# Performance work log

Hardware: AMD Instinct MI355X
Metric: run time of the kernel (lower is better)

Reference implementation:

```python
import jax, jax.numpy as jnp
from jax import lax
import numpy as np

B, C_IN, C_OUT, T, N, E = 4, 32, 32, 48, 2000, 16000


def _tconv(x, w, b):
    # Conv2d with kernel (3,1), padding (1,0): temporal conv over T, per-node.
    y = lax.conv_general_dilated(x, w, window_strides=(1, 1),
                                 padding=((1, 1), (0, 0)),
                                 dimension_numbers=('NCHW', 'OIHW', 'NCHW'))
    return y + b[None, :, None, None]


def setup_inputs() -> dict:
    key = jax.random.key(0)
    ks = jax.random.split(key, 8)
    x = jax.random.normal(ks[0], (B, C_IN, T, N), dtype=jnp.float32)
    edge_index = jax.random.randint(ks[1], (2, E), 0, N, dtype=jnp.int64)
    w1 = jax.random.normal(ks[2], (C_OUT, C_IN, 3, 1), dtype=jnp.float32) * 0.05
    b1 = jnp.zeros((C_OUT,), dtype=jnp.float32)
    gcn_w = jax.random.normal(ks[3], (C_OUT, C_OUT), dtype=jnp.float32) * 0.05
    gcn_b = jnp.zeros((C_OUT,), dtype=jnp.float32)
    w2 = jax.random.normal(ks[4], (C_OUT, C_OUT, 3, 1), dtype=jnp.float32) * 0.05
    b2 = jnp.zeros((C_OUT,), dtype=jnp.float32)
    return {"x": x, "edge_index": edge_index, "w1": w1, "b1": b1,
            "gcn_w": gcn_w, "gcn_b": gcn_b, "w2": w2, "b2": b2}


def reference(x, edge_index, w1, b1, gcn_w, gcn_b, w2, b2):
    # temporal conv 1 + relu
    h = jax.nn.relu(_tconv(x, w1, b1))          # [B, C, T, N]
    Bs, C, Ts, Ns = h.shape
    # replicate-graph GCN: same edge_index for all B*T graphs
    xf = h.transpose(0, 2, 3, 1).reshape(Bs * Ts, Ns, C)   # [BT, N, C]
    xw = xf @ gcn_w                                        # linear transform first
    src, dst = edge_index[0], edge_index[1]
    # GCN symmetric normalization with self-loops: deg = 1 + in-degree
    deg = jnp.zeros((Ns,), xw.dtype).at[dst].add(1.0) + 1.0
    dinv = lax.rsqrt(deg)
    wedge = dinv[src] * dinv[dst]                           # [E]

    def aggregate(g):  # g: [N, C] for one graph
        return jnp.zeros((Ns, C), g.dtype).at[dst].add(g[src] * wedge[:, None])

    agg = jax.vmap(aggregate)(xw)                           # [BT, N, C]
    out = agg + (1.0 / deg)[None, :, None] * xw + gcn_b     # self-loop term + bias
    out = out.reshape(Bs, Ts, Ns, C).transpose(0, 3, 1, 2)  # [B, C, T, N]
    # temporal conv 2
    return _tconv(out, w2, b2)
```

## Files before the change

### kernel.cpp

```cpp
#include <hip/hip_runtime.h>

#define BB 4
#define CIN 32
#define COUT 32
#define TT 48
#define NN 2000
#define EE 16000
#define BT (BB*TT)
#define PADCOL 24576
#define NGB 24


__global__ __launch_bounds__(1024) void k_build(
        const int* __restrict__ ei,
        const float* __restrict__ w1, const float* __restrict__ gw,
        const float* __restrict__ gb, const float* __restrict__ w2,
        int* __restrict__ rowptr, float* __restrict__ dinv2,
        int* __restrict__ col, float* __restrict__ wedge,
        float* __restrict__ w1t, float* __restrict__ w2c,
        float* __restrict__ bias2) {
    __shared__ int   cnt[2048];
    __shared__ int   buf[2048];
    __shared__ float sdinv[2048];
    __shared__ float sw2t[3072];
    __shared__ float sgw[1024];
    int t = threadIdx.x;

    for (int i = t; i < 3072; i += 1024) {
        int c = i & 31, r = i >> 5;
        int co = r & 31, k = r >> 5;
        sw2t[i] = w2[c * 96 + co * 3 + k];
        w1t[i]  = w1[c * 96 + co * 3 + k];
    }
    sgw[t] = gw[t];
    cnt[t] = 0; cnt[t + 1024] = 0;
    __syncthreads();

    for (int e = t; e < EE; e += 1024) atomicAdd(&cnt[ei[EE + e]], 1);
    __syncthreads();

    for (int i = t; i < 2048; i += 1024)
        buf[i] = (i < NN) ? ((cnt[i] + 3) & ~3) : 0;
    __syncthreads();
    for (int s = 1; s < 2048; s <<= 1) {
        int i0 = t, i1 = t + 1024;
        int a0 = buf[i0] + ((i0 >= s) ? buf[i0 - s] : 0);
        int a1 = buf[i1] + ((i1 >= s) ? buf[i1 - s] : 0);
        __syncthreads();
        buf[i0] = a0; buf[i1] = a1;
        __syncthreads();
    }

    for (int i = t; i < 2048; i += 1024) {
        if (i < NN) {
            rowptr[i + 1] = buf[i];
            float deg = (float)(cnt[i] + 1);
            sdinv[i] = rsqrtf(deg);
            dinv2[i] = 1.0f / deg;
        }
    }
    if (t == 0) rowptr[0] = 0;
    __syncthreads();

    int P = buf[NN - 1];
    for (int i = t; i < P; i += 1024) { col[i] = 0; wedge[i] = 0.f; }
    for (int i = t; i < NN; i += 1024)
        cnt[i] = buf[i] - ((cnt[i] + 3) & ~3);
    __syncthreads();

    for (int e = t; e < EE; e += 1024) {
        int s = ei[e], d = ei[EE + e];
        int pos = atomicAdd(&cnt[d], 1);
        col[pos]   = s;
        wedge[pos] = sdinv[s] * sdinv[d];
    }

    for (int i = t; i < 3072; i += 1024) {
        int c = i & 31, r = i >> 5;
        int cm = r & 31, k = r >> 5;
        float acc = 0.f;
#pragma unroll
        for (int co = 0; co < 32; co++)
            acc += sgw[cm * 32 + co] * sw2t[(k * 32 + co) * 32 + c];
        w2c[i] = acc;
    }
    for (int i = t; i < 96; i += 1024) {
        int k = i >> 5, c = i & 31;
        float acc = 0.f;
#pragma unroll
        for (int co = 0; co < 32; co++)
            acc += gb[co] * sw2t[(k * 32 + co) * 32 + c];
        bias2[i] = acc;
    }
}


__global__ __launch_bounds__(256) void k_conv1(const float* __restrict__ x,
                                               const float* __restrict__ w1t,
                                               const float* __restrict__ b1,
                                               float* __restrict__ hbuf) {
    int idx = blockIdx.x * 256 + threadIdx.x;
    int n0 = idx * 2;
    if (n0 >= NN) return;
    int t = blockIdx.y, b = blockIdx.z;
    int g = b * TT + t;
    int gb = g >> 3, gsub = g & 7;

    float ha[COUT], hb[COUT];
#pragma unroll
    for (int c = 0; c < COUT; c++) { ha[c] = b1[c]; hb[c] = b1[c]; }

    for (int k = 0; k < 3; k++) {
        int tt = t + k - 1;
        if (tt < 0 || tt >= TT) continue;
        const float* xb = x + (((size_t)b * CIN) * TT + tt) * NN + n0;
        const float* wp = w1t + k * CIN * COUT;
#pragma unroll
        for (int ci = 0; ci < CIN; ci++) {
            float2 xv = *(const float2*)(xb + (size_t)ci * TT * NN);
#pragma unroll
            for (int c = 0; c < COUT; c++) {
                float wv = wp[ci * COUT + c];
                ha[c] += xv.x * wv;
                hb[c] += xv.y * wv;
            }
        }
    }

    float4* pa = (float4*)(hbuf + (((size_t)gb * NN + n0) * 8 + gsub) * 32);
    float4* pb = (float4*)(hbuf + (((size_t)gb * NN + n0 + 1) * 8 + gsub) * 32);
#pragma unroll
    for (int q = 0; q < 8; q++) {
        pa[q] = make_float4(fmaxf(ha[4*q], 0.f), fmaxf(ha[4*q+1], 0.f),
                            fmaxf(ha[4*q+2], 0.f), fmaxf(ha[4*q+3], 0.f));
        pb[q] = make_float4(fmaxf(hb[4*q], 0.f), fmaxf(hb[4*q+1], 0.f),
                            fmaxf(hb[4*q+2], 0.f), fmaxf(hb[4*q+3], 0.f));
    }
}


__global__ __launch_bounds__(256) void k_agg(const float* __restrict__ hbuf,
                                             const int* __restrict__ rowptr,
                                             const int* __restrict__ col,
                                             const float* __restrict__ wedge,
                                             const float* __restrict__ dinv2,
                                             float* __restrict__ gbuf) {
    int bid = blockIdx.x;
    int xcd = bid & 7;
    int q   = bid >> 3;
    int gbr = q / 500;
    int nch = q % 500;
    int gb  = gbr * 8 + xcd;
    int wid  = threadIdx.x >> 6;
    int lane = threadIdx.x & 63;
    int gsub = lane >> 3;
    int cq   = lane & 7;
    int n    = nch * 4 + wid;

    const float* xg = hbuf + (size_t)gb * NN * 256;
    size_t loff = (size_t)gsub * 32 + cq * 4;

    float4 self = *(const float4*)(xg + (size_t)n * 256 + loff);
    float dv = dinv2[n];
    float4 acc = make_float4(dv * self.x, dv * self.y, dv * self.z, dv * self.w);

    int j  = rowptr[n];
    int je = rowptr[n + 1];
    for (; j < je; j += 4) {
        int4   cc = *(const int4*)(col + j);
        float4 ww = *(const float4*)(wedge + j);
        float4 v0 = *(const float4*)(xg + (size_t)cc.x * 256 + loff);
        float4 v1 = *(const float4*)(xg + (size_t)cc.y * 256 + loff);
        float4 v2 = *(const float4*)(xg + (size_t)cc.z * 256 + loff);
        float4 v3 = *(const float4*)(xg + (size_t)cc.w * 256 + loff);
        acc.x += ww.x*v0.x + ww.y*v1.x + ww.z*v2.x + ww.w*v3.x;
        acc.y += ww.x*v0.y + ww.y*v1.y + ww.z*v2.y + ww.w*v3.y;
        acc.z += ww.x*v0.z + ww.y*v1.z + ww.z*v2.z + ww.w*v3.z;
        acc.w += ww.x*v0.w + ww.y*v1.w + ww.z*v2.w + ww.w*v3.w;
    }

    int g = gb * 8 + gsub;
    *(float4*)(gbuf + ((size_t)g * NN + n) * 32 + cq * 4) = acc;
}


__global__ __launch_bounds__(256) void k_conv2(const float* __restrict__ gbuf,
                                               const float* __restrict__ w2c,
                                               const float* __restrict__ bias2,
                                               const float* __restrict__ b2,
                                               float* __restrict__ out) {
    int n = blockIdx.x * 256 + threadIdx.x;
    if (n >= NN) return;
    int t = blockIdx.y, b = blockIdx.z;

    float o[COUT];
#pragma unroll
    for (int c = 0; c < COUT; c++) o[c] = b2[c];

    for (int k = 0; k < 3; k++) {
        int tt = t + k - 1;
        if (tt < 0 || tt >= TT) continue;
        const float4* gp = (const float4*)(gbuf + (((size_t)(b * TT + tt)) * NN + n) * CIN);
        const float* wp = w2c + k * CIN * COUT;
        const float* bp = bias2 + k * COUT;
        float gv[CIN];
#pragma unroll
        for (int qq = 0; qq < 8; qq++) {
            float4 v = gp[qq];
            gv[4*qq] = v.x; gv[4*qq+1] = v.y; gv[4*qq+2] = v.z; gv[4*qq+3] = v.w;
        }
#pragma unroll
        for (int c = 0; c < COUT; c++) o[c] += bp[c];
#pragma unroll
        for (int cm = 0; cm < CIN; cm++) {
#pragma unroll
            for (int c = 0; c < COUT; c++) o[c] += gv[cm] * wp[cm * COUT + c];
        }
    }

#pragma unroll
    for (int c = 0; c < COUT; c++)
        out[(((size_t)b * COUT + c) * TT + t) * NN + n] = o[c];
}


extern "C" void kernel_launch(void* const* d_in, const int* in_sizes, int n_in,
                              void* d_out, int out_size, void* d_ws, size_t ws_size,
                              hipStream_t stream) {
    const float* x     = (const float*)d_in[0];
    const int*   ei    = (const int*)d_in[1];
    const float* w1    = (const float*)d_in[2];
    const float* b1    = (const float*)d_in[3];
    const float* gcn_w = (const float*)d_in[4];
    const float* gcn_b = (const float*)d_in[5];
    const float* w2    = (const float*)d_in[6];
    const float* b2    = (const float*)d_in[7];
    float* out = (float*)d_out;

    const size_t XWB = (size_t)BT * NN * COUT * sizeof(float);
    char* w = (char*)d_ws;
    float* hbuf   = (float*)w;  w += XWB;
    float* gbuf   = (float*)w;  w += XWB;
    int*   rowptr = (int*)w;    w += 8192;
    float* dinv2  = (float*)w;  w += 8192;
    int*   col    = (int*)w;    w += PADCOL * sizeof(int);
    float* wedge  = (float*)w;  w += PADCOL * sizeof(float);
    float* w1t    = (float*)w;  w += 3072 * sizeof(float);
    float* w2c    = (float*)w;  w += 3072 * sizeof(float);
    float* bias2  = (float*)w;  w += 96 * sizeof(float);

    k_build<<<dim3(1), dim3(1024), 0, stream>>>(ei, w1, gcn_w, gcn_b, w2,
                                                rowptr, dinv2, col, wedge,
                                                w1t, w2c, bias2);
    k_conv1<<<dim3(4, TT, BB), dim3(256), 0, stream>>>(x, w1t, b1, hbuf);
    k_agg  <<<dim3(12000), dim3(256), 0, stream>>>(hbuf, rowptr, col, wedge, dinv2, gbuf);
    k_conv2<<<dim3(8, TT, BB), dim3(256), 0, stream>>>(gbuf, w2c, bias2, b2, out);
}
```

Before: 269.1 us.

## Move CSR edge fill to a parallel kernel and use one node per conv1 thread

The edge scatter that fills col/wedge moves out of the single-block build kernel into a separate multi-block kernel that uses global atomics on a fill pointer. The aim is to shorten the serial single-workgroup setup phase. Conv1 now has each thread compute one node instead of two and launches twice as many blocks, which raises parallelism and lowers register pressure but drops the float2 loads. The change adds one kernel launch, and the global atomics make the edge order within each row nondeterministic, as it already was.

```diff
diff --git a/kernel.cpp b/kernel.cpp
--- a/kernel.cpp
+++ b/kernel.cpp
@@ -8,7 +8,6 @@
 #define EE 16000
 #define BT (BB*TT)
 #define PADCOL 24576
-#define NGB 24
 
 
 __global__ __launch_bounds__(1024) void k_build(
@@ -16,12 +15,12 @@
         const float* __restrict__ w1, const float* __restrict__ gw,
         const float* __restrict__ gb, const float* __restrict__ w2,
         int* __restrict__ rowptr, float* __restrict__ dinv2,
+        float* __restrict__ dinvg, int* __restrict__ fillptr,
         int* __restrict__ col, float* __restrict__ wedge,
         float* __restrict__ w1t, float* __restrict__ w2c,
         float* __restrict__ bias2) {
     __shared__ int   cnt[2048];
     __shared__ int   buf[2048];
-    __shared__ float sdinv[2048];
     __shared__ float sw2t[3072];
     __shared__ float sgw[1024];
     int t = threadIdx.x;
@@ -55,25 +54,16 @@
         if (i < NN) {
             rowptr[i + 1] = buf[i];
             float deg = (float)(cnt[i] + 1);
-            sdinv[i] = rsqrtf(deg);
+            dinvg[i] = rsqrtf(deg);
             dinv2[i] = 1.0f / deg;
+            fillptr[i] = buf[i] - ((cnt[i] + 3) & ~3);
         }
     }
     if (t == 0) rowptr[0] = 0;
-    __syncthreads();
 
     int P = buf[NN - 1];
+    __syncthreads();
     for (int i = t; i < P; i += 1024) { col[i] = 0; wedge[i] = 0.f; }
-    for (int i = t; i < NN; i += 1024)
-        cnt[i] = buf[i] - ((cnt[i] + 3) & ~3);
-    __syncthreads();
-
-    for (int e = t; e < EE; e += 1024) {
-        int s = ei[e], d = ei[EE + e];
-        int pos = atomicAdd(&cnt[d], 1);
-        col[pos]   = s;
-        wedge[pos] = sdinv[s] * sdinv[d];
-    }
 
     for (int i = t; i < 3072; i += 1024) {
         int c = i & 31, r = i >> 5;
@@ -95,47 +85,51 @@
 }
 
 
+__global__ void k_fill(const int* __restrict__ ei, int* __restrict__ fillptr,
+                       const float* __restrict__ dinvg,
+                       int* __restrict__ col, float* __restrict__ wedge) {
+    int e = blockIdx.x * blockDim.x + threadIdx.x;
+    if (e < EE) {
+        int s = ei[e], d = ei[EE + e];
+        int pos = atomicAdd(fillptr + d, 1);
+        col[pos]   = s;
+        wedge[pos] = dinvg[s] * dinvg[d];
+    }
+}
+
+
 __global__ __launch_bounds__(256) void k_conv1(const float* __restrict__ x,
                                                const float* __restrict__ w1t,
                                                const float* __restrict__ b1,
                                                float* __restrict__ hbuf) {
-    int idx = blockIdx.x * 256 + threadIdx.x;
-    int n0 = idx * 2;
-    if (n0 >= NN) return;
+    int n = blockIdx.x * 256 + threadIdx.x;
+    if (n >= NN) return;
     int t = blockIdx.y, b = blockIdx.z;
     int g = b * TT + t;
     int gb = g >> 3, gsub = g & 7;
 
-    float ha[COUT], hb[COUT];
-#pragma unroll
-    for (int c = 0; c < COUT; c++) { ha[c] = b1[c]; hb[c] = b1[c]; }
+    float ha[COUT];
+#pragma unroll
+    for (int c = 0; c < COUT; c++) ha[c] = b1[c];
 
     for (int k = 0; k < 3; k++) {
         int tt = t + k - 1;
         if (tt < 0 || tt >= TT) continue;
-        const float* xb = x + (((size_t)b * CIN) * TT + tt) * NN + n0;
+        const float* xb = x + (((size_t)b * CIN) * TT + tt) * NN + n;
         const float* wp = w1t + k * CIN * COUT;
 #pragma unroll
         for (int ci = 0; ci < CIN; ci++) {
-            float2 xv = *(const float2*)(xb + (size_t)ci * TT * NN);
-#pragma unroll
-            for (int c = 0; c < COUT; c++) {
-                float wv = wp[ci * COUT + c];
-                ha[c] += xv.x * wv;
-                hb[c] += xv.y * wv;
-            }
-        }
-    }
-
-    float4* pa = (float4*)(hbuf + (((size_t)gb * NN + n0) * 8 + gsub) * 32);
-    float4* pb = (float4*)(hbuf + (((size_t)gb * NN + n0 + 1) * 8 + gsub) * 32);
-#pragma unroll
-    for (int q = 0; q < 8; q++) {
+            float xv = xb[(size_t)ci * TT * NN];
+#pragma unroll
+            for (int c = 0; c < COUT; c++) ha[c] += xv * wp[ci * COUT + c];
+        }
+    }
+
+    float4* pa = (float4*)(hbuf + (((size_t)gb * NN + n) * 8 + gsub) * 32);
+#pragma unroll
+    for (int q = 0; q < 8; q++)
         pa[q] = make_float4(fmaxf(ha[4*q], 0.f), fmaxf(ha[4*q+1], 0.f),
                             fmaxf(ha[4*q+2], 0.f), fmaxf(ha[4*q+3], 0.f));
-        pb[q] = make_float4(fmaxf(hb[4*q], 0.f), fmaxf(hb[4*q+1], 0.f),
-                            fmaxf(hb[4*q+2], 0.f), fmaxf(hb[4*q+3], 0.f));
-    }
 }
 
 
@@ -239,20 +233,23 @@
 
     const size_t XWB = (size_t)BT * NN * COUT * sizeof(float);
     char* w = (char*)d_ws;
-    float* hbuf   = (float*)w;  w += XWB;
-    float* gbuf   = (float*)w;  w += XWB;
-    int*   rowptr = (int*)w;    w += 8192;
-    float* dinv2  = (float*)w;  w += 8192;
-    int*   col    = (int*)w;    w += PADCOL * sizeof(int);
-    float* wedge  = (float*)w;  w += PADCOL * sizeof(float);
-    float* w1t    = (float*)w;  w += 3072 * sizeof(float);
-    float* w2c    = (float*)w;  w += 3072 * sizeof(float);
-    float* bias2  = (float*)w;  w += 96 * sizeof(float);
+    float* hbuf    = (float*)w;  w += XWB;
+    float* gbuf    = (float*)w;  w += XWB;
+    int*   rowptr  = (int*)w;    w += 8192;
+    float* dinv2   = (float*)w;  w += 8192;
+    float* dinvg   = (float*)w;  w += 8192;
+    int*   fillptr = (int*)w;    w += 8192;
+    int*   col     = (int*)w;    w += PADCOL * sizeof(int);
+    float* wedge   = (float*)w;  w += PADCOL * sizeof(float);
+    float* w1t     = (float*)w;  w += 3072 * sizeof(float);
+    float* w2c     = (float*)w;  w += 3072 * sizeof(float);
+    float* bias2   = (float*)w;  w += 96 * sizeof(float);
 
     k_build<<<dim3(1), dim3(1024), 0, stream>>>(ei, w1, gcn_w, gcn_b, w2,
-                                                rowptr, dinv2, col, wedge,
-                                                w1t, w2c, bias2);
-    k_conv1<<<dim3(4, TT, BB), dim3(256), 0, stream>>>(x, w1t, b1, hbuf);
+                                                rowptr, dinv2, dinvg, fillptr,
+                                                col, wedge, w1t, w2c, bias2);
+    k_fill <<<dim3((EE + 255) / 256), dim3(256), 0, stream>>>(ei, fillptr, dinvg, col, wedge);
+    k_conv1<<<dim3(8, TT, BB), dim3(256), 0, stream>>>(x, w1t, b1, hbuf);
     k_agg  <<<dim3(12000), dim3(256), 0, stream>>>(hbuf, rowptr, col, wedge, dinv2, gbuf);
     k_conv2<<<dim3(8, TT, BB), dim3(256), 0, stream>>>(gbuf, w2c, bias2, b2, out);
 }
```

After: 257.4 us. 1.05x faster.
